# Kernel tuning notes

Measured on AMD Instinct MI355X. Metric: run time of the kernel, lower is better.

Reference implementation:

```python
import jax, jax.numpy as jnp
import numpy as np

B, N, F = 2, 512, 128
NEG_SLOPE = 0.04
MASK_VAL = -9.0e15


def setup_inputs() -> dict:
    key = jax.random.key(0)
    ks = jax.random.split(key, 5)
    x = jax.random.normal(ks[0], (B, N, F), dtype=jnp.float32)
    adj = jax.random.randint(ks[1], (B, N, N), 0, 2, dtype=jnp.int32)
    s1 = 1.0 / np.sqrt(2 * F)
    # mlp(2F, [2F, 1], last_relu=False): Linear(2F,2F) -> ReLU -> Linear(2F,1)
    w1 = (jax.random.normal(ks[2], (2 * F, 2 * F), dtype=jnp.float32) * s1)
    b1 = jnp.zeros((2 * F,), dtype=jnp.float32)
    w2 = (jax.random.normal(ks[3], (1, 2 * F), dtype=jnp.float32) * s1)
    b2 = jnp.zeros((1,), dtype=jnp.float32)
    return {"x": x, "w1": w1, "b1": b1, "w2": w2, "b2": b2, "adj": adj}


def reference(x, w1, b1, w2, b2, adj):
    f = x.shape[-1]
    # concat(X_i, X_j) @ W1^T == X_i @ W1[:, :F]^T + X_j @ W1[:, F:]^T
    w1a, w1b = w1[:, :f], w1[:, f:]
    p = jnp.einsum('bnf,hf->bnh', x, w1a)          # [B,N,2F]  (i-part)
    q = jnp.einsum('bnf,hf->bnh', x, w1b)          # [B,N,2F]  (j-part)
    h = jax.nn.relu(p[:, :, None, :] + q[:, None, :, :] + b1)  # [B,N,N,2F]
    e = jnp.einsum('bijh,oh->bij', h, w2) + b2[0]  # [B,N,N] edge logits
    # LeakyReLU(negative_slope=0.04)
    e = jnp.where(e > 0, e, NEG_SLOPE * e)
    e = jnp.where(adj > 0, e, MASK_VAL)
    attention = jax.nn.softmax(e, axis=2)          # [B,N,N]
    next_h = jnp.einsum('bij,bjf->bif', attention, x)  # [B,N,F]
    return next_h, attention[0, 0, :]
```

## Files before the change

### kernel.cpp

```cpp
#include <hip/hip_runtime.h>

#define BB 2
#define NN 512
#define FF 128
#define HH 256
#define TI 4

#define K1_BN 256
#define K1_HT 8
#define K1_FC 32

__global__ __launch_bounds__(256) void k1_pq(const float* __restrict__ x,
    const float* __restrict__ w1, const float* __restrict__ b1,
    float* __restrict__ s_out, float* __restrict__ qT) {
  __shared__ float x_l[K1_BN][K1_FC + 1];
  const int t   = threadIdx.x;
  const int bn0 = blockIdx.x * K1_BN;
  const int h0  = blockIdx.y * K1_HT;
  const bool qhalf = (h0 >= HH);
  const int wbase  = qhalf ? ((h0 - HH) * (2 * FF) + FF) : (h0 * (2 * FF));

  float acc[K1_HT];
  #pragma unroll
  for (int k = 0; k < K1_HT; ++k) acc[k] = 0.f;

  for (int fc = 0; fc < FF; fc += K1_FC) {
    __syncthreads();
    {
      const int r0 = t >> 3, fq = (t & 7) * 4;
      #pragma unroll
      for (int rr = 0; rr < K1_BN; rr += 32) {
        float4 v = *(const float4*)(x + (bn0 + r0 + rr) * FF + fc + fq);
        x_l[r0 + rr][fq]     = v.x;
        x_l[r0 + rr][fq + 1] = v.y;
        x_l[r0 + rr][fq + 2] = v.z;
        x_l[r0 + rr][fq + 3] = v.w;
      }
    }
    __syncthreads();
    #pragma unroll 4
    for (int f = 0; f < K1_FC; ++f) {
      float xv = x_l[t][f];
      #pragma unroll
      for (int k = 0; k < K1_HT; ++k) {
        float wv = w1[wbase + k * (2 * FF) + fc + f];
        acc[k] = fmaf(xv, wv, acc[k]);
      }
    }
  }

  const int bn = bn0 + t;
  if (!qhalf) {
    #pragma unroll
    for (int k = 0; k < K1_HT; ++k) acc[k] += b1[h0 + k];
    float4 o0 = make_float4(acc[0], acc[1], acc[2], acc[3]);
    float4 o1 = make_float4(acc[4], acc[5], acc[6], acc[7]);
    *(float4*)(s_out + bn * HH + h0)     = o0;
    *(float4*)(s_out + bn * HH + h0 + 4) = o1;
  } else {
    #pragma unroll
    for (int k = 0; k < K1_HT; ++k)
      qT[(h0 - HH + k) * (BB * NN) + bn] = acc[k];
  }
}

__global__ __launch_bounds__(512) void k2_attn(const float* __restrict__ s,
    const float* __restrict__ qT, const float* __restrict__ x,
    const float* __restrict__ w2, const float* __restrict__ b2,
    const int* __restrict__ adj, float* __restrict__ out) {
  __shared__ __align__(16) float e_l[TI][NN];
  __shared__ __align__(16) float part_l[8][TI][FF];
  __shared__ float red_m[TI][2];
  __shared__ float red_s[TI][2];

  const int blk = blockIdx.x;
  const int b   = blk >> 7;
  const int i0  = (blk & 127) * TI;
  const int t   = threadIdx.x;
  const int wv  = t >> 6, ln = t & 63;
  const int j   = wv * 64 + ln;

  {
    const float* s0   = s + (b * NN + i0) * HH;
    const float* qcol = qT + b * NN + j;
    float a0 = 0.f, a1 = 0.f, a2 = 0.f, a3 = 0.f;
    #pragma unroll 4
    for (int h = 0; h < HH; ++h) {
      float qv = qcol[h * (BB * NN)];
      float wh = w2[h];
      a0 = fmaf(fmaxf(s0[h]          + qv, 0.f), wh, a0);
      a1 = fmaf(fmaxf(s0[HH + h]     + qv, 0.f), wh, a1);
      a2 = fmaf(fmaxf(s0[2 * HH + h] + qv, 0.f), wh, a2);
      a3 = fmaf(fmaxf(s0[3 * HH + h] + qv, 0.f), wh, a3);
    }
    const float b2v = b2[0];
    const int* arow = adj + (b * NN + i0) * NN + j;
    float e;
    e = a0 + b2v; e = e > 0.f ? e : 0.04f * e; e_l[0][j] = (arow[0]      > 0) ? e : -9.0e15f;
    e = a1 + b2v; e = e > 0.f ? e : 0.04f * e; e_l[1][j] = (arow[NN]     > 0) ? e : -9.0e15f;
    e = a2 + b2v; e = e > 0.f ? e : 0.04f * e; e_l[2][j] = (arow[2 * NN] > 0) ? e : -9.0e15f;
    e = a3 + b2v; e = e > 0.f ? e : 0.04f * e; e_l[3][j] = (arow[3 * NN] > 0) ? e : -9.0e15f;
  }
  __syncthreads();

  {
    const int ti = wv & 3, hf = wv >> 2;
    float4 v = *(float4*)&e_l[ti][hf * 256 + 4 * ln];
    float m = fmaxf(fmaxf(v.x, v.y), fmaxf(v.z, v.w));
    #pragma unroll
    for (int off = 32; off > 0; off >>= 1) m = fmaxf(m, __shfl_xor(m, off, 64));
    if (ln == 0) red_m[ti][hf] = m;
    __syncthreads();
    m = fmaxf(red_m[ti][0], red_m[ti][1]);
    v.x = __expf(v.x - m); v.y = __expf(v.y - m);
    v.z = __expf(v.z - m); v.w = __expf(v.w - m);
    float zs = (v.x + v.y) + (v.z + v.w);
    #pragma unroll
    for (int off = 32; off > 0; off >>= 1) zs += __shfl_xor(zs, off, 64);
    if (ln == 0) red_s[ti][hf] = zs;
    __syncthreads();
    float inv = 1.f / (red_s[ti][0] + red_s[ti][1]);
    v.x *= inv; v.y *= inv; v.z *= inv; v.w *= inv;
    *(float4*)&e_l[ti][hf * 256 + 4 * ln] = v;
  }
  __syncthreads();

  if (blk == 0) out[BB * NN * FF + t] = e_l[0][t];

  {
    const int hf = ln >> 5;
    const int fq = (ln & 31) * 4;
    const int jb = wv * 64 + hf * 32;
    float4 acc[TI];
    #pragma unroll
    for (int ti = 0; ti < TI; ++ti) acc[ti] = make_float4(0.f, 0.f, 0.f, 0.f);

    for (int s8 = 0; s8 < 8; ++s8) {
      const int j0 = jb + s8 * 4;
      float4 aa[TI];
      #pragma unroll
      for (int ti = 0; ti < TI; ++ti) aa[ti] = *(float4*)&e_l[ti][j0];
      #pragma unroll
      for (int jj = 0; jj < 4; ++jj) {
        float4 xv = *(const float4*)(x + (b * NN + j0 + jj) * FF + fq);
        #pragma unroll
        for (int ti = 0; ti < TI; ++ti) {
          float w = (jj == 0) ? aa[ti].x : (jj == 1) ? aa[ti].y : (jj == 2) ? aa[ti].z : aa[ti].w;
          acc[ti].x = fmaf(w, xv.x, acc[ti].x);
          acc[ti].y = fmaf(w, xv.y, acc[ti].y);
          acc[ti].z = fmaf(w, xv.z, acc[ti].z);
          acc[ti].w = fmaf(w, xv.w, acc[ti].w);
        }
      }
    }
    #pragma unroll
    for (int ti = 0; ti < TI; ++ti) {
      acc[ti].x += __shfl_xor(acc[ti].x, 32, 64);
      acc[ti].y += __shfl_xor(acc[ti].y, 32, 64);
      acc[ti].z += __shfl_xor(acc[ti].z, 32, 64);
      acc[ti].w += __shfl_xor(acc[ti].w, 32, 64);
    }
    if (ln < 32) {
      #pragma unroll
      for (int ti = 0; ti < TI; ++ti)
        *(float4*)&part_l[wv][ti][fq] = acc[ti];
    }
  }
  __syncthreads();
  {
    const int ti = t >> 7, f = t & 127;
    float r = 0.f;
    #pragma unroll
    for (int w = 0; w < 8; ++w) r += part_l[w][ti][f];
    out[(b * NN + i0 + ti) * FF + f] = r;
  }
}

extern "C" void kernel_launch(void* const* d_in, const int* in_sizes, int n_in,
                              void* d_out, int out_size, void* d_ws, size_t ws_size,
                              hipStream_t stream) {
  const float* x   = (const float*)d_in[0];
  const float* w1  = (const float*)d_in[1];
  const float* b1  = (const float*)d_in[2];
  const float* w2  = (const float*)d_in[3];
  const float* b2  = (const float*)d_in[4];
  const int*   adj = (const int*)  d_in[5];
  float* out = (float*)d_out;

  float* s  = (float*)d_ws;
  float* qT = s + BB * NN * HH;

  dim3 g1(BB * NN / K1_BN, (2 * HH) / K1_HT);
  k1_pq  <<<g1, K1_BN, 0, stream>>>(x, w1, b1, s, qT);
  k2_attn<<<BB * NN / TI, 512, 0, stream>>>(s, qT, x, w2, b2, adj, out);
}
```

Measured before the change: 105.8 us.

## Rework projection kernel tiling and split attention hidden dim across 1024-thread blocks

The first kernel now stages 64 rows of W1 in shared memory with a rotated layout and has each wave compute 4 nodes against 64 hidden units. Its q half is transposed through shared memory so qT stores coalesce. The attention kernel doubles block size to 1024 threads and splits the 256-wide hidden reduction into two halves whose partial sums are combined in shared memory. This adds parallelism to the dominant edge-logit loop at the cost of extra LDS traffic and one more barrier. Softmax and the aggregation step are remapped so each wave handles one row and a quarter of the neighbours.

Measured after the change: 93.32 us. 1.13x faster.

```diff
diff --git a/kernel.cpp b/kernel.cpp
--- a/kernel.cpp
+++ b/kernel.cpp
@@ -6,172 +6,175 @@
 #define HH 256
 #define TI 4
 
-#define K1_BN 256
-#define K1_HT 8
-#define K1_FC 32
-
 __global__ __launch_bounds__(256) void k1_pq(const float* __restrict__ x,
     const float* __restrict__ w1, const float* __restrict__ b1,
     float* __restrict__ s_out, float* __restrict__ qT) {
-  __shared__ float x_l[K1_BN][K1_FC + 1];
+  __shared__ __align__(16) float w1_l[64][FF];
+  __shared__ float qtmp[64][17];
   const int t   = threadIdx.x;
-  const int bn0 = blockIdx.x * K1_BN;
-  const int h0  = blockIdx.y * K1_HT;
-  const bool qhalf = (h0 >= HH);
-  const int wbase  = qhalf ? ((h0 - HH) * (2 * FF) + FF) : (h0 * (2 * FF));
+  const int bn0 = blockIdx.x * 16;
+  const int h0  = blockIdx.y * 64;
+  const bool qh = (h0 >= HH);
+  const int rowbase = qh ? (h0 - HH) : h0;
+  const int colbase = qh ? FF : 0;
 
-  float acc[K1_HT];
   #pragma unroll
-  for (int k = 0; k < K1_HT; ++k) acc[k] = 0.f;
+  for (int k = 0; k < 8; ++k) {
+    int idx = t + 256 * k;
+    int r = idx >> 5, c4 = (idx & 31) * 4;
+    float4 v = *(const float4*)(w1 + (rowbase + r) * (2 * FF) + colbase + c4);
+    *(float4*)&w1_l[r][(c4 + 4 * r) & 127] = v;
+  }
+  __syncthreads();
 
-  for (int fc = 0; fc < FF; fc += K1_FC) {
-    __syncthreads();
-    {
-      const int r0 = t >> 3, fq = (t & 7) * 4;
-      #pragma unroll
-      for (int rr = 0; rr < K1_BN; rr += 32) {
-        float4 v = *(const float4*)(x + (bn0 + r0 + rr) * FF + fc + fq);
-        x_l[r0 + rr][fq]     = v.x;
-        x_l[r0 + rr][fq + 1] = v.y;
-        x_l[r0 + rr][fq + 2] = v.z;
-        x_l[r0 + rr][fq + 3] = v.w;
-      }
-    }
-    __syncthreads();
-    #pragma unroll 4
-    for (int f = 0; f < K1_FC; ++f) {
-      float xv = x_l[t][f];
-      #pragma unroll
-      for (int k = 0; k < K1_HT; ++k) {
-        float wv = w1[wbase + k * (2 * FF) + fc + f];
-        acc[k] = fmaf(xv, wv, acc[k]);
-      }
-    }
+  const int l  = t & 63;
+  const int sb = __builtin_amdgcn_readfirstlane(t >> 6);
+  const float* xr = x + (bn0 + sb * 4) * FF;
+  float acc0 = 0.f, acc1 = 0.f, acc2 = 0.f, acc3 = 0.f;
+
+  #pragma unroll 4
+  for (int f4 = 0; f4 < FF; f4 += 4) {
+    float4 wv = *(float4*)&w1_l[l][(f4 + 4 * l) & 127];
+    float4 x0 = *(const float4*)(xr + f4);
+    float4 x1 = *(const float4*)(xr + FF + f4);
+    float4 x2 = *(const float4*)(xr + 2 * FF + f4);
+    float4 x3 = *(const float4*)(xr + 3 * FF + f4);
+    acc0 = fmaf(x0.x, wv.x, acc0); acc0 = fmaf(x0.y, wv.y, acc0);
+    acc0 = fmaf(x0.z, wv.z, acc0); acc0 = fmaf(x0.w, wv.w, acc0);
+    acc1 = fmaf(x1.x, wv.x, acc1); acc1 = fmaf(x1.y, wv.y, acc1);
+    acc1 = fmaf(x1.z, wv.z, acc1); acc1 = fmaf(x1.w, wv.w, acc1);
+    acc2 = fmaf(x2.x, wv.x, acc2); acc2 = fmaf(x2.y, wv.y, acc2);
+    acc2 = fmaf(x2.z, wv.z, acc2); acc2 = fmaf(x2.w, wv.w, acc2);
+    acc3 = fmaf(x3.x, wv.x, acc3); acc3 = fmaf(x3.y, wv.y, acc3);
+    acc3 = fmaf(x3.z, wv.z, acc3); acc3 = fmaf(x3.w, wv.w, acc3);
   }
 
-  const int bn = bn0 + t;
-  if (!qhalf) {
+  const int bn = bn0 + sb * 4;
+  if (!qh) {
+    float bv = b1[h0 + l];
+    s_out[(bn    ) * HH + h0 + l] = acc0 + bv;
+    s_out[(bn + 1) * HH + h0 + l] = acc1 + bv;
+    s_out[(bn + 2) * HH + h0 + l] = acc2 + bv;
+    s_out[(bn + 3) * HH + h0 + l] = acc3 + bv;
+  } else {
+    qtmp[l][sb * 4]     = acc0;
+    qtmp[l][sb * 4 + 1] = acc1;
+    qtmp[l][sb * 4 + 2] = acc2;
+    qtmp[l][sb * 4 + 3] = acc3;
+    __syncthreads();
     #pragma unroll
-    for (int k = 0; k < K1_HT; ++k) acc[k] += b1[h0 + k];
-    float4 o0 = make_float4(acc[0], acc[1], acc[2], acc[3]);
-    float4 o1 = make_float4(acc[4], acc[5], acc[6], acc[7]);
-    *(float4*)(s_out + bn * HH + h0)     = o0;
-    *(float4*)(s_out + bn * HH + h0 + 4) = o1;
-  } else {
-    #pragma unroll
-    for (int k = 0; k < K1_HT; ++k)
-      qT[(h0 - HH + k) * (BB * NN) + bn] = acc[k];
+    for (int k = 0; k < 4; ++k) {
+      int idx = t + 256 * k;
+      int r = idx >> 4, c = idx & 15;
+      qT[(h0 - HH + r) * (BB * NN) + bn0 + c] = qtmp[r][c];
+    }
   }
 }
 
-__global__ __launch_bounds__(512) void k2_attn(const float* __restrict__ s,
+__global__ __launch_bounds__(1024) void k2_attn(const float* __restrict__ s,
     const float* __restrict__ qT, const float* __restrict__ x,
     const float* __restrict__ w2, const float* __restrict__ b2,
     const int* __restrict__ adj, float* __restrict__ out) {
   __shared__ __align__(16) float e_l[TI][NN];
-  __shared__ __align__(16) float part_l[8][TI][FF];
-  __shared__ float red_m[TI][2];
-  __shared__ float red_s[TI][2];
+  __shared__ __align__(16) float pe[2][TI][NN];
+  __shared__ __align__(16) float part_l[4][TI][FF];
+  __shared__ float red_m[TI][4];
+  __shared__ float red_s[TI][4];
 
   const int blk = blockIdx.x;
   const int b   = blk >> 7;
   const int i0  = (blk & 127) * TI;
   const int t   = threadIdx.x;
-  const int wv  = t >> 6, ln = t & 63;
-  const int j   = wv * 64 + ln;
+  const int wv  = __builtin_amdgcn_readfirstlane(t >> 6);
+  const int ln  = t & 63;
 
   {
-    const float* s0   = s + (b * NN + i0) * HH;
-    const float* qcol = qT + b * NN + j;
+    const int hg = wv >> 3;
+    const int j  = (wv & 7) * 64 + ln;
+    const float* qcol = qT + hg * 128 * (BB * NN) + b * NN + j;
+    const float* s0   = s + (b * NN + i0) * HH + hg * 128;
+    const float* w2p  = w2 + hg * 128;
     float a0 = 0.f, a1 = 0.f, a2 = 0.f, a3 = 0.f;
-    #pragma unroll 4
-    for (int h = 0; h < HH; ++h) {
+    #pragma unroll 8
+    for (int h = 0; h < 128; ++h) {
       float qv = qcol[h * (BB * NN)];
-      float wh = w2[h];
+      float wh = w2p[h];
       a0 = fmaf(fmaxf(s0[h]          + qv, 0.f), wh, a0);
       a1 = fmaf(fmaxf(s0[HH + h]     + qv, 0.f), wh, a1);
       a2 = fmaf(fmaxf(s0[2 * HH + h] + qv, 0.f), wh, a2);
       a3 = fmaf(fmaxf(s0[3 * HH + h] + qv, 0.f), wh, a3);
     }
-    const float b2v = b2[0];
-    const int* arow = adj + (b * NN + i0) * NN + j;
-    float e;
-    e = a0 + b2v; e = e > 0.f ? e : 0.04f * e; e_l[0][j] = (arow[0]      > 0) ? e : -9.0e15f;
-    e = a1 + b2v; e = e > 0.f ? e : 0.04f * e; e_l[1][j] = (arow[NN]     > 0) ? e : -9.0e15f;
-    e = a2 + b2v; e = e > 0.f ? e : 0.04f * e; e_l[2][j] = (arow[2 * NN] > 0) ? e : -9.0e15f;
-    e = a3 + b2v; e = e > 0.f ? e : 0.04f * e; e_l[3][j] = (arow[3 * NN] > 0) ? e : -9.0e15f;
+    pe[hg][0][j] = a0; pe[hg][1][j] = a1;
+    pe[hg][2][j] = a2; pe[hg][3][j] = a3;
   }
   __syncthreads();
 
   {
-    const int ti = wv & 3, hf = wv >> 2;
-    float4 v = *(float4*)&e_l[ti][hf * 256 + 4 * ln];
-    float m = fmaxf(fmaxf(v.x, v.y), fmaxf(v.z, v.w));
+    const float b2v = b2[0];
     #pragma unroll
-    for (int off = 32; off > 0; off >>= 1) m = fmaxf(m, __shfl_xor(m, off, 64));
-    if (ln == 0) red_m[ti][hf] = m;
-    __syncthreads();
-    m = fmaxf(red_m[ti][0], red_m[ti][1]);
-    v.x = __expf(v.x - m); v.y = __expf(v.y - m);
-    v.z = __expf(v.z - m); v.w = __expf(v.w - m);
-    float zs = (v.x + v.y) + (v.z + v.w);
-    #pragma unroll
-    for (int off = 32; off > 0; off >>= 1) zs += __shfl_xor(zs, off, 64);
-    if (ln == 0) red_s[ti][hf] = zs;
-    __syncthreads();
-    float inv = 1.f / (red_s[ti][0] + red_s[ti][1]);
-    v.x *= inv; v.y *= inv; v.z *= inv; v.w *= inv;
-    *(float4*)&e_l[ti][hf * 256 + 4 * ln] = v;
+    for (int r = 0; r < 2; ++r) {
+      int idx = t + 1024 * r;
+      int ti = idx >> 9, j2 = idx & 511;
+      float e = pe[0][ti][j2] + pe[1][ti][j2] + b2v;
+      e = e > 0.f ? e : 0.04f * e;
+      int av = adj[(b * NN + i0 + ti) * NN + j2];
+      e_l[ti][j2] = (av > 0) ? e : -9.0e15f;
+    }
   }
   __syncthreads();
 
-  if (blk == 0) out[BB * NN * FF + t] = e_l[0][t];
+  {
+    const int ti = wv >> 2, qtr = wv & 3;
+    float2 v = *(float2*)&e_l[ti][qtr * 128 + 2 * ln];
+    float m = fmaxf(v.x, v.y);
+    #pragma unroll
+    for (int off = 32; off > 0; off >>= 1) m = fmaxf(m, __shfl_xor(m, off, 64));
+    if (ln == 0) red_m[ti][qtr] = m;
+    __syncthreads();
+    m = fmaxf(fmaxf(red_m[ti][0], red_m[ti][1]), fmaxf(red_m[ti][2], red_m[ti][3]));
+    v.x = __expf(v.x - m); v.y = __expf(v.y - m);
+    float zs = v.x + v.y;
+    #pragma unroll
+    for (int off = 32; off > 0; off >>= 1) zs += __shfl_xor(zs, off, 64);
+    if (ln == 0) red_s[ti][qtr] = zs;
+    __syncthreads();
+    float inv = 1.f / ((red_s[ti][0] + red_s[ti][1]) + (red_s[ti][2] + red_s[ti][3]));
+    v.x *= inv; v.y *= inv;
+    *(float2*)&e_l[ti][qtr * 128 + 2 * ln] = v;
+  }
+  __syncthreads();
+
+  if (blk == 0 && t < NN) out[BB * NN * FF + t] = e_l[0][t];
 
   {
-    const int hf = ln >> 5;
-    const int fq = (ln & 31) * 4;
-    const int jb = wv * 64 + hf * 32;
-    float4 acc[TI];
-    #pragma unroll
-    for (int ti = 0; ti < TI; ++ti) acc[ti] = make_float4(0.f, 0.f, 0.f, 0.f);
-
-    for (int s8 = 0; s8 < 8; ++s8) {
-      const int j0 = jb + s8 * 4;
-      float4 aa[TI];
-      #pragma unroll
-      for (int ti = 0; ti < TI; ++ti) aa[ti] = *(float4*)&e_l[ti][j0];
+    const int ti = wv & 3, qtr = wv >> 2;
+    const int jh = ln >> 5, fq = (ln & 31) * 4;
+    const int jb = qtr * 128 + jh * 64;
+    float4 acc = make_float4(0.f, 0.f, 0.f, 0.f);
+    for (int s4 = 0; s4 < 16; ++s4) {
+      const int j0 = jb + s4 * 4;
+      float4 aa = *(float4*)&e_l[ti][j0];
       #pragma unroll
       for (int jj = 0; jj < 4; ++jj) {
         float4 xv = *(const float4*)(x + (b * NN + j0 + jj) * FF + fq);
-        #pragma unroll
-        for (int ti = 0; ti < TI; ++ti) {
-          float w = (jj == 0) ? aa[ti].x : (jj == 1) ? aa[ti].y : (jj == 2) ? aa[ti].z : aa[ti].w;
-          acc[ti].x = fmaf(w, xv.x, acc[ti].x);
-          acc[ti].y = fmaf(w, xv.y, acc[ti].y);
-          acc[ti].z = fmaf(w, xv.z, acc[ti].z);
-          acc[ti].w = fmaf(w, xv.w, acc[ti].w);
-        }
+        float w = (jj == 0) ? aa.x : (jj == 1) ? aa.y : (jj == 2) ? aa.z : aa.w;
+        acc.x = fmaf(w, xv.x, acc.x);
+        acc.y = fmaf(w, xv.y, acc.y);
+        acc.z = fmaf(w, xv.z, acc.z);
+        acc.w = fmaf(w, xv.w, acc.w);
       }
     }
-    #pragma unroll
-    for (int ti = 0; ti < TI; ++ti) {
-      acc[ti].x += __shfl_xor(acc[ti].x, 32, 64);
-      acc[ti].y += __shfl_xor(acc[ti].y, 32, 64);
-      acc[ti].z += __shfl_xor(acc[ti].z, 32, 64);
-      acc[ti].w += __shfl_xor(acc[ti].w, 32, 64);
-    }
-    if (ln < 32) {
-      #pragma unroll
-      for (int ti = 0; ti < TI; ++ti)
-        *(float4*)&part_l[wv][ti][fq] = acc[ti];
-    }
+    acc.x += __shfl_xor(acc.x, 32, 64);
+    acc.y += __shfl_xor(acc.y, 32, 64);
+    acc.z += __shfl_xor(acc.z, 32, 64);
+    acc.w += __shfl_xor(acc.w, 32, 64);
+    if (ln < 32) *(float4*)&part_l[qtr][ti][fq] = acc;
   }
   __syncthreads();
-  {
+  if (t < TI * FF) {
     const int ti = t >> 7, f = t & 127;
-    float r = 0.f;
-    #pragma unroll
-    for (int w = 0; w < 8; ++w) r += part_l[w][ti][f];
+    float r = (part_l[0][ti][f] + part_l[1][ti][f])
+            + (part_l[2][ti][f] + part_l[3][ti][f]);
     out[(b * NN + i0 + ti) * FF + f] = r;
   }
 }
@@ -190,7 +193,7 @@
   float* s  = (float*)d_ws;
   float* qT = s + BB * NN * HH;
 
-  dim3 g1(BB * NN / K1_BN, (2 * HH) / K1_HT);
-  k1_pq  <<<g1, K1_BN, 0, stream>>>(x, w1, b1, s, qT);
-  k2_attn<<<BB * NN / TI, 512, 0, stream>>>(s, qT, x, w2, b2, adj, out);
+  dim3 g1(BB * NN / 16, (2 * HH) / 64);
+  k1_pq  <<<g1, 256, 0, stream>>>(x, w1, b1, s, qT);
+  k2_attn<<<BB * NN / TI, 1024, 0, stream>>>(s, qT, x, w2, b2, adj, out);
 }
```
